# Performance work log

Hardware: AMD Instinct MI355X
Metric: run time of the kernel (lower is better)

## Reference

```python
import jax, jax.numpy as jnp
import numpy as np

SEQ, IN, H = 8192, 1024, 2048

def setup_inputs() -> dict:
    key = jax.random.key(0)
    ks = jax.random.split(key, 7)
    s = 0.02
    return {
        "input_seq": jax.random.normal(ks[0], (SEQ, IN), jnp.float32),
        "W_ih": jax.random.normal(ks[1], (4 * H, IN), jnp.float32) * s,
        "W_hh": jax.random.normal(ks[2], (4 * H, H), jnp.float32) * s,
        "b_ih": jax.random.normal(ks[3], (4 * H,), jnp.float32) * s,
        "b_hh": jax.random.normal(ks[4], (4 * H,), jnpp if False else jnp.float32) * s if False else jax.random.normal(ks[4], (4 * H,), jnp.float32) * s,
        "W_lin": jax.random.normal(ks[5], (1, H), jnp.float32) * s,
        "b_lin": jax.random.normal(ks[6], (1,), jnp.float32) * s,
    }

def _lstm(input_seq, W_ih, W_hh, b, H):
    # Precompute input projections for all timesteps: [S, 4H]
    x_proj = input_seq @ W_ih.T + b

    def step(carry, xp):
        h, c = carry
        gates = xp + h @ W_hh.T  # [4H], PyTorch order: i, f, g, o
        i = jax.nn.sigmoid(gates[0:H])
        f = jax.nn.sigmoid(gates[H:2 * H])
        g = jnp.tanh(gates[2 * H:3 * H])
        o = jax.nn.sigmoid(gates[3 * H:4 * H])
        c = f * c + i * g
        h = o * jnp.tanh(c)
        return (h, c), h

    h0 = jnp.zeros((H,), input_seq.dtype)
    c0 = jnp.zeros((H,), input_seq.dtype)
    _, hs = jax.lax.scan(step, (h0, c0), x_proj)
    return hs  # [S, H]

def reference(input_seq, W_ih, W_hh, b_ih, b_hh, W_lin, b_lin):
    H_ = W_hh.shape[1]
    hs = _lstm(input_seq, W_ih, W_hh, b_ih + b_hh, H_)
    # dropout is identity in eval mode; then linear + sigmoid + flatten
    out = jax.nn.sigmoid(hs @ W_lin.T + b_lin)  # [S, 1]
    return out.reshape(-1)
```

## Files before the change

kernel.cpp:

```cpp
#include <hip/hip_runtime.h>
#include <hip/hip_bf16.h>
#include <stdint.h>

constexpr int kSEQ = 8192;
constexpr int kIN  = 1024;
constexpr int kH   = 2048;
constexpr int kG4  = 4 * kH;
constexpr int kNB  = 256;
constexpr int kHB  = kH / kNB;
constexpr int kWP  = kH + 16;

constexpr size_t OFF_HBUF  = 0;
constexpr size_t OFF_ABORT = 32768;
constexpr size_t OFF_HS    = 65536;
constexpr size_t OFF_XP    = OFF_HS + (size_t)kSEQ * kH * 2;

__device__ __forceinline__ float bflo(uint32_t v) { return __uint_as_float(v << 16); }
__device__ __forceinline__ float bfhi(uint32_t v) { return __uint_as_float(v & 0xffff0000u); }

__global__ __launch_bounds__(256) void k_xproj(const float* __restrict__ A,
                                               const float* __restrict__ B,
                                               const float* __restrict__ bih,
                                               const float* __restrict__ bhh,
                                               __hip_bfloat16* __restrict__ C)
{
    __shared__ float As[16][65];
    __shared__ float Bs[16][65];

    const int bx = blockIdx.x & 127;
    const int by = blockIdx.x >> 7;
    const int tid = threadIdx.x;
    const int r  = tid >> 2;
    const int kq = (tid & 3) << 2;
    const int tx = tid & 15;
    const int ty = tid >> 4;
    const int m0 = by * 64, n0 = bx * 64;

    float acc[4][4] = {};

    for (int k0 = 0; k0 < kIN; k0 += 16) {
        float4 av = *(const float4*)&A[(size_t)(m0 + r) * kIN + k0 + kq];
        float4 bv = *(const float4*)&B[(size_t)(n0 + r) * kIN + k0 + kq];
        __syncthreads();
        As[kq + 0][r] = av.x; As[kq + 1][r] = av.y; As[kq + 2][r] = av.z; As[kq + 3][r] = av.w;
        Bs[kq + 0][r] = bv.x; Bs[kq + 1][r] = bv.y; Bs[kq + 2][r] = bv.z; Bs[kq + 3][r] = bv.w;
        __syncthreads();
        #pragma unroll
        for (int k = 0; k < 16; ++k) {
            float a0 = As[k][ty * 4 + 0], a1 = As[k][ty * 4 + 1];
            float a2 = As[k][ty * 4 + 2], a3 = As[k][ty * 4 + 3];
            float b0 = Bs[k][tx * 4 + 0], b1 = Bs[k][tx * 4 + 1];
            float b2 = Bs[k][tx * 4 + 2], b3 = Bs[k][tx * 4 + 3];
            acc[0][0] += a0 * b0; acc[0][1] += a0 * b1; acc[0][2] += a0 * b2; acc[0][3] += a0 * b3;
            acc[1][0] += a1 * b0; acc[1][1] += a1 * b1; acc[1][2] += a1 * b2; acc[1][3] += a1 * b3;
            acc[2][0] += a2 * b0; acc[2][1] += a2 * b1; acc[2][2] += a2 * b2; acc[2][3] += a2 * b3;
            acc[3][0] += a3 * b0; acc[3][1] += a3 * b1; acc[3][2] += a3 * b2; acc[3][3] += a3 * b3;
        }
    }

    #pragma unroll
    for (int i = 0; i < 4; ++i) {
        const int m = m0 + ty * 4 + i;
        #pragma unroll
        for (int j = 0; j < 4; ++j) {
            const int n = n0 + tx * 4 + j;
            C[(size_t)m * kG4 + n] = __float2bfloat16(acc[i][j] + bih[n] + bhh[n]);
        }
    }
}

__global__ __launch_bounds__(256, 1) void k_lstm(const float* __restrict__ Whh,
                                                 const __hip_bfloat16* __restrict__ xp,
                                                 unsigned long long* __restrict__ hbuf,
                                                 uint32_t* __restrict__ abortf,
                                                 __hip_bfloat16* __restrict__ hs)
{
    extern __shared__ char smem[];
    __hip_bfloat16* Wl   = (__hip_bfloat16*)smem;
    float*          hl   = (float*)(smem + 32 * kWP * 2);
    float*          gbuf = (float*)(smem + 32 * kWP * 2 + kH * 4);
    float*          xbuf = gbuf + 32;

    const int wg  = blockIdx.x;
    const int tid = threadIdx.x;
    const int w   = tid >> 6;
    const int l   = tid & 63;
    const int hb  = wg * kHB;

    {
        const int lr = tid >> 3;
        const int g  = lr >> 3, j = lr & 7;
        const int cb = (tid & 7) * 256;
        const float* src = Whh + (size_t)(g * kH + hb + j) * kH + cb;
        __hip_bfloat16* dst = Wl + (size_t)lr * kWP + cb;
        for (int c = 0; c < 256; c += 4) {
            float4 v = *(const float4*)(src + c);
            dst[c + 0] = __float2bfloat16(v.x);
            dst[c + 1] = __float2bfloat16(v.y);
            dst[c + 2] = __float2bfloat16(v.z);
            dst[c + 3] = __float2bfloat16(v.w);
        }
    }
    __syncthreads();

    float c_state = 0.0f;
    const __hip_bfloat16* wrow = Wl + (size_t)(w * 8 + (l >> 3)) * kWP;
    const int kbase = (l & 7) * 8;
    uint32_t budget = 0;

    for (int t = 0; t < kSEQ; ++t) {
        float xv = 0.f;
        if (tid < 32)
            xv = __bfloat162float(xp[(size_t)t * kG4 + (tid >> 3) * kH + hb + (tid & 7)]);

        int dead = 0;
        if (t == 0) {
            float* d = hl + tid * 8;
            #pragma unroll
            for (int j = 0; j < 8; ++j) d[j] = 0.f;
        } else {
            const unsigned long long* src = hbuf + (size_t)((t - 1) & 1) * kH + tid * 8;
            const uint32_t tag = (uint32_t)t;
            float* d = hl + tid * 8;
            #pragma unroll 1
            for (int j = 0; j < 8 && !dead; ++j) {
                unsigned long long v;
                for (;;) {
                    v = __hip_atomic_load(src + j, __ATOMIC_RELAXED, __HIP_MEMORY_SCOPE_AGENT);
                    if ((uint32_t)v == tag) break;
                    if ((++budget & 1023) == 0) {
                        if (__hip_atomic_load(abortf, __ATOMIC_RELAXED,
                                              __HIP_MEMORY_SCOPE_AGENT) != 0u) { dead = 1; break; }
                        if (budget > (1u << 22)) {
                            __hip_atomic_store(abortf, 1u, __ATOMIC_RELAXED,
                                               __HIP_MEMORY_SCOPE_AGENT);
                            dead = 1; break;
                        }
                    }
                }
                d[j] = __uint_as_float((uint32_t)(v >> 32));
            }
        }
        if (tid < 32) xbuf[tid] = xv;
        if (__syncthreads_or(dead)) return;

        float acc = 0.f;
        #pragma unroll 8
        for (int it = 0; it < 32; ++it) {
            const int k = it * 64 + kbase;
            uint4 wv = *(const uint4*)(wrow + k);
            float4 h0 = *(const float4*)(hl + k);
            float4 h1 = *(const float4*)(hl + k + 4);
            acc += bflo(wv.x) * h0.x + bfhi(wv.x) * h0.y
                 + bflo(wv.y) * h0.z + bfhi(wv.y) * h0.w
                 + bflo(wv.z) * h1.x + bfhi(wv.z) * h1.y
                 + bflo(wv.w) * h1.z + bfhi(wv.w) * h1.w;
        }
        acc += __shfl_xor(acc, 1);
        acc += __shfl_xor(acc, 2);
        acc += __shfl_xor(acc, 4);
        if ((l & 7) == 0) gbuf[w * 8 + (l >> 3)] = acc;
        __syncthreads();

        if (tid < 8) {
            const int j = tid;
            const float gi = gbuf[0 * 8 + j] + xbuf[0 * 8 + j];
            const float gf = gbuf[1 * 8 + j] + xbuf[1 * 8 + j];
            const float gg = gbuf[2 * 8 + j] + xbuf[2 * 8 + j];
            const float go = gbuf[3 * 8 + j] + xbuf[3 * 8 + j];
            const float si = 1.f / (1.f + expf(-gi));
            const float sf = 1.f / (1.f + expf(-gf));
            const float tg = tanhf(gg);
            const float so = 1.f / (1.f + expf(-go));
            c_state = sf * c_state + si * tg;
            const float hv = so * tanhf(c_state);
            hs[(size_t)t * kH + hb + j] = __float2bfloat16(hv);
            const unsigned long long pv =
                ((unsigned long long)__float_as_uint(hv) << 32) | (uint32_t)(t + 1);
            __hip_atomic_store(hbuf + (size_t)(t & 1) * kH + hb + j, pv,
                               __ATOMIC_RELAXED, __HIP_MEMORY_SCOPE_AGENT);
        }
    }
}

__global__ __launch_bounds__(256) void k_out(const __hip_bfloat16* __restrict__ hs,
                                             const float* __restrict__ wlin,
                                             const float* __restrict__ blin,
                                             float* __restrict__ out)
{
    const int w = threadIdx.x >> 6, l = threadIdx.x & 63;
    const int t = blockIdx.x * 4 + w;
    const __hip_bfloat16* row = hs + (size_t)t * kH;
    float acc = 0.f;
    #pragma unroll
    for (int i = 0; i < 4; ++i) {
        const int k = i * 512 + l * 8;
        uint4 hv = *(const uint4*)(row + k);
        float4 w0 = *(const float4*)(wlin + k);
        float4 w1 = *(const float4*)(wlin + k + 4);
        acc += bflo(hv.x) * w0.x + bfhi(hv.x) * w0.y
             + bflo(hv.y) * w0.z + bfhi(hv.y) * w0.w
             + bflo(hv.z) * w1.x + bfhi(hv.z) * w1.y
             + bflo(hv.w) * w1.z + bfhi(hv.w) * w1.w;
    }
    #pragma unroll
    for (int s = 32; s >= 1; s >>= 1) acc += __shfl_xor(acc, s);
    if (l == 0) out[t] = 1.f / (1.f + expf(-(acc + blin[0])));
}

extern "C" void kernel_launch(void* const* d_in, const int* in_sizes, int n_in,
                              void* d_out, int out_size, void* d_ws, size_t ws_size,
                              hipStream_t stream)
{
    const float* input_seq = (const float*)d_in[0];
    const float* W_ih      = (const float*)d_in[1];
    const float* W_hh      = (const float*)d_in[2];
    const float* b_ih      = (const float*)d_in[3];
    const float* b_hh      = (const float*)d_in[4];
    const float* W_lin     = (const float*)d_in[5];
    const float* b_lin     = (const float*)d_in[6];
    float* out = (float*)d_out;
    char*  ws  = (char*)d_ws;

    unsigned long long* hbuf = (unsigned long long*)(ws + OFF_HBUF);
    uint32_t*           abf  = (uint32_t*)(ws + OFF_ABORT);
    __hip_bfloat16*     hs   = (__hip_bfloat16*)(ws + OFF_HS);
    __hip_bfloat16*     xpb  = (__hip_bfloat16*)(ws + OFF_XP);

    hipMemsetAsync(ws, 0, 65536, stream);

    k_xproj<<<dim3(128 * 128), dim3(256), 0, stream>>>(input_seq, W_ih, b_ih, b_hh, xpb);

    constexpr int kLds = 32 * kWP * 2 + kH * 4 + 64 * 4;
    hipFuncSetAttribute((const void*)k_lstm, hipFuncAttributeMaxDynamicSharedMemorySize, kLds);

    {
        const float* a0 = W_hh; const __hip_bfloat16* a1 = xpb;
        unsigned long long* a2 = hbuf; uint32_t* a3 = abf; __hip_bfloat16* a4 = hs;
        void* args[5] = { &a0, &a1, &a2, &a3, &a4 };
        hipError_t ce = hipLaunchCooperativeKernel((const void*)k_lstm, dim3(kNB), dim3(256),
                                                   args, (unsigned)kLds, stream);
        if (ce != hipSuccess) {
            k_lstm<<<dim3(kNB), dim3(256), kLds, stream>>>(W_hh, xpb, hbuf, abf, hs);
        }
    }

    k_out<<<dim3(kSEQ / 4), dim3(256), 0, stream>>>(hs, W_lin, b_lin, out);
}
```

Baseline: 55.08 ms.

## Remove per-step block barrier by reordering gate rows and double-buffering h in LDS

Permutes the W_hh rows staged in LDS so that the four gates for one hidden unit land inside a single half-wavefront. Gate values are then gathered with shuffles and the LSTM cell update runs in registers, removing the second __syncthreads and the gbuf/xbuf round trip through shared memory. The h vector in LDS is double-buffered so the next step's writes cannot race with readers of the current one. The spin-wait now polls all 8 flags in one batch per round instead of one flag at a time, and checks the abort flag more often. The cost is redundant gate math on every lane and extra global loads of the x projection on every thread.

```diff
diff --git a/kernel.cpp b/kernel.cpp
--- a/kernel.cpp
+++ b/kernel.cpp
@@ -76,10 +76,8 @@
                                                  __hip_bfloat16* __restrict__ hs)
 {
     extern __shared__ char smem[];
-    __hip_bfloat16* Wl   = (__hip_bfloat16*)smem;
-    float*          hl   = (float*)(smem + 32 * kWP * 2);
-    float*          gbuf = (float*)(smem + 32 * kWP * 2 + kH * 4);
-    float*          xbuf = gbuf + 32;
+    __hip_bfloat16* Wl  = (__hip_bfloat16*)smem;
+    float*          hl2 = (float*)(smem + 32 * kWP * 2);
 
     const int wg  = blockIdx.x;
     const int tid = threadIdx.x;
@@ -89,9 +87,10 @@
 
     {
         const int lr = tid >> 3;
-        const int g  = lr >> 3, j = lr & 7;
+        const int g  = lr & 3;
+        const int jl = 2 * (lr >> 3) + ((lr >> 2) & 1);
         const int cb = (tid & 7) * 256;
-        const float* src = Whh + (size_t)(g * kH + hb + j) * kH + cb;
+        const float* src = Whh + (size_t)(g * kH + hb + jl) * kH + cb;
         __hip_bfloat16* dst = Wl + (size_t)lr * kWP + cb;
         for (int c = 0; c < 256; c += 4) {
             float4 v = *(const float4*)(src + c);
@@ -103,54 +102,59 @@
     }
     __syncthreads();
 
-    float c_state = 0.0f;
     const __hip_bfloat16* wrow = Wl + (size_t)(w * 8 + (l >> 3)) * kWP;
     const int kbase = (l & 7) * 8;
+    const int jg = hb + 2 * w + (l >> 5);
+    float c_state = 0.0f;
     uint32_t budget = 0;
 
     for (int t = 0; t < kSEQ; ++t) {
-        float xv = 0.f;
-        if (tid < 32)
-            xv = __bfloat162float(xp[(size_t)t * kG4 + (tid >> 3) * kH + hb + (tid & 7)]);
-
+        const __hip_bfloat16* xr = xp + (size_t)t * kG4 + jg;
+        const float xi = __bfloat162float(xr[0]);
+        const float xf = __bfloat162float(xr[kH]);
+        const float xg = __bfloat162float(xr[2 * kH]);
+        const float xo = __bfloat162float(xr[3 * kH]);
+
+        float* hw = hl2 + (size_t)(t & 1) * kH + tid * 8;
         int dead = 0;
         if (t == 0) {
-            float* d = hl + tid * 8;
             #pragma unroll
-            for (int j = 0; j < 8; ++j) d[j] = 0.f;
+            for (int j = 0; j < 8; ++j) hw[j] = 0.f;
         } else {
             const unsigned long long* src = hbuf + (size_t)((t - 1) & 1) * kH + tid * 8;
             const uint32_t tag = (uint32_t)t;
-            float* d = hl + tid * 8;
-            #pragma unroll 1
-            for (int j = 0; j < 8 && !dead; ++j) {
-                unsigned long long v;
-                for (;;) {
-                    v = __hip_atomic_load(src + j, __ATOMIC_RELAXED, __HIP_MEMORY_SCOPE_AGENT);
-                    if ((uint32_t)v == tag) break;
-                    if ((++budget & 1023) == 0) {
-                        if (__hip_atomic_load(abortf, __ATOMIC_RELAXED,
-                                              __HIP_MEMORY_SCOPE_AGENT) != 0u) { dead = 1; break; }
-                        if (budget > (1u << 22)) {
-                            __hip_atomic_store(abortf, 1u, __ATOMIC_RELAXED,
-                                               __HIP_MEMORY_SCOPE_AGENT);
-                            dead = 1; break;
-                        }
+            unsigned long long v[8];
+            for (;;) {
+                #pragma unroll
+                for (int j = 0; j < 8; ++j)
+                    v[j] = __hip_atomic_load(src + j, __ATOMIC_RELAXED, __HIP_MEMORY_SCOPE_AGENT);
+                bool ok = true;
+                #pragma unroll
+                for (int j = 0; j < 8; ++j) ok &= ((uint32_t)v[j] == tag);
+                if (ok) break;
+                if ((++budget & 15) == 0) {
+                    if (__hip_atomic_load(abortf, __ATOMIC_RELAXED,
+                                          __HIP_MEMORY_SCOPE_AGENT) != 0u) { dead = 1; break; }
+                    if (budget > (1u << 21)) {
+                        __hip_atomic_store(abortf, 1u, __ATOMIC_RELAXED,
+                                           __HIP_MEMORY_SCOPE_AGENT);
+                        dead = 1; break;
                     }
                 }
-                d[j] = __uint_as_float((uint32_t)(v >> 32));
             }
-        }
-        if (tid < 32) xbuf[tid] = xv;
+            #pragma unroll
+            for (int j = 0; j < 8; ++j) hw[j] = __uint_as_float((uint32_t)(v[j] >> 32));
+        }
         if (__syncthreads_or(dead)) return;
 
+        const float* hv = hl2 + (size_t)(t & 1) * kH;
         float acc = 0.f;
         #pragma unroll 8
         for (int it = 0; it < 32; ++it) {
             const int k = it * 64 + kbase;
             uint4 wv = *(const uint4*)(wrow + k);
-            float4 h0 = *(const float4*)(hl + k);
-            float4 h1 = *(const float4*)(hl + k + 4);
+            float4 h0 = *(const float4*)(hv + k);
+            float4 h1 = *(const float4*)(hv + k + 4);
             acc += bflo(wv.x) * h0.x + bfhi(wv.x) * h0.y
                  + bflo(wv.y) * h0.z + bfhi(wv.y) * h0.w
                  + bflo(wv.z) * h1.x + bfhi(wv.z) * h1.y
@@ -159,25 +163,23 @@
         acc += __shfl_xor(acc, 1);
         acc += __shfl_xor(acc, 2);
         acc += __shfl_xor(acc, 4);
-        if ((l & 7) == 0) gbuf[w * 8 + (l >> 3)] = acc;
-        __syncthreads();
-
-        if (tid < 8) {
-            const int j = tid;
-            const float gi = gbuf[0 * 8 + j] + xbuf[0 * 8 + j];
-            const float gf = gbuf[1 * 8 + j] + xbuf[1 * 8 + j];
-            const float gg = gbuf[2 * 8 + j] + xbuf[2 * 8 + j];
-            const float go = gbuf[3 * 8 + j] + xbuf[3 * 8 + j];
-            const float si = 1.f / (1.f + expf(-gi));
-            const float sf = 1.f / (1.f + expf(-gf));
-            const float tg = tanhf(gg);
-            const float so = 1.f / (1.f + expf(-go));
-            c_state = sf * c_state + si * tg;
-            const float hv = so * tanhf(c_state);
-            hs[(size_t)t * kH + hb + j] = __float2bfloat16(hv);
+
+        const int base = l & 32;
+        const float gi = __shfl(acc, base + 0)  + xi;
+        const float gf = __shfl(acc, base + 8)  + xf;
+        const float gg = __shfl(acc, base + 16) + xg;
+        const float go = __shfl(acc, base + 24) + xo;
+        const float si = 1.f / (1.f + expf(-gi));
+        const float sf = 1.f / (1.f + expf(-gf));
+        const float tg = tanhf(gg);
+        const float so = 1.f / (1.f + expf(-go));
+        c_state = sf * c_state + si * tg;
+        const float hvv = so * tanhf(c_state);
+        if ((l & 31) == 0) {
+            hs[(size_t)t * kH + jg] = __float2bfloat16(hvv);
             const unsigned long long pv =
-                ((unsigned long long)__float_as_uint(hv) << 32) | (uint32_t)(t + 1);
-            __hip_atomic_store(hbuf + (size_t)(t & 1) * kH + hb + j, pv,
+                ((unsigned long long)__float_as_uint(hvv) << 32) | (uint32_t)(t + 1);
+            __hip_atomic_store(hbuf + (size_t)(t & 1) * kH + jg, pv,
                                __ATOMIC_RELAXED, __HIP_MEMORY_SCOPE_AGENT);
         }
     }
@@ -231,7 +233,7 @@
 
     k_xproj<<<dim3(128 * 128), dim3(256), 0, stream>>>(input_seq, W_ih, b_ih, b_hh, xpb);
 
-    constexpr int kLds = 32 * kWP * 2 + kH * 4 + 64 * 4;
+    constexpr int kLds = 32 * kWP * 2 + 2 * kH * 4;
     hipFuncSetAttribute((const void*)k_lstm, hipFuncAttributeMaxDynamicSharedMemorySize, kLds);
 
     {
```

Result: slower. 60.05 ms (+9.0%).
